# Kernel optimization log

Measured on AMD Instinct MI355X. Metric: run time of the kernel, lower is better.

The kernel has to match this reference:

```python
import jax, jax.numpy as jnp
import numpy as np

IN_F, H1, H2, OUT_F = 16, 512, 1024, 16
N_NODES, N_EDGES = 20000, 160000


def gcn_conv(x, src, dst, W, b, n):
    # PyG GCNConv: add self-loops, symmetric deg^-1/2 normalization,
    # linear transform first, then normalized scatter-add aggregation.
    loop = jnp.arange(n, dtype=src.dtype)
    s = jnp.concatenate([src, loop])
    d = jnp.concatenate([dst, loop])
    deg = jax.ops.segment_sum(jnp.ones(s.shape[0], x.dtype), d, num_segments=n)
    dinv = jnp.where(deg > 0, jax.lax.rsqrt(deg), 0.0)
    h = x @ W                      # [n, out]
    norm = dinv[s] * dinv[d]       # [e]
    msg = h[s] * norm[:, None]     # [e, out]
    return jax.ops.segment_sum(msg, d, num_segments=n) + b


def setup_inputs() -> dict:
    key = jax.random.key(0)
    ks = jax.random.split(key, 8)
    node_matrix = jax.random.normal(ks[0], (N_NODES, IN_F), dtype=jnp.float32)
    graph = jax.random.randint(ks[1], (2, N_EDGES), 0, N_NODES, dtype=jnp.int64)
    def glorot(k, shape):
        lim = np.sqrt(6.0 / (shape[0] + shape[1]))
        return jax.random.uniform(k, shape, jnp.float32, -lim, lim)
    return {
        "node_matrix": node_matrix,
        "graph": graph,
        "W1": glorot(ks[2], (IN_F, H1)),
        "b1": jnp.zeros((H1,), jnp.float32),
        "W2": glorot(ks[3], (H1, H2)),
        "b2": jnp.zeros((H2,), jnp.float32),
        "Wl": glorot(ks[4], (H2, OUT_F)),
        "bl": jnp.zeros((OUT_F,), jnp.float32),
    }


def reference(node_matrix, graph, W1, b1, W2, b2, Wl, bl):
    n = node_matrix.shape[0]
    src, dst = graph[0], graph[1]
    x = gcn_conv(node_matrix, src, dst, W1, b1, n)
    x = jax.nn.relu(x)
    # dropout is identity in eval mode
    x = gcn_conv(x, src, dst, W2, b2, n)
    return x @ Wl + bl
```

## Files before the change

### kernel.cpp

```cpp
#include <hip/hip_runtime.h>


constexpr int IN_F  = 16;
constexpr int H1D   = 512;
constexpr int H2D   = 1024;
constexpr int OUTF  = 16;
constexpr int PAD   = 64;

__global__ void k_prep(int* __restrict__ counts, float* __restrict__ WfB,
                       float* __restrict__ bf, float* __restrict__ W1T,
                       const float* __restrict__ W1, const float* __restrict__ W2,
                       const float* __restrict__ Wl, const float* __restrict__ b2,
                       const float* __restrict__ bl, int n) {
  int b = blockIdx.x, tid = threadIdx.x;
  if (b < 32) {
    int g = b * 256 + tid;
    int j = g >> 4, o = g & 15;
    const float* w2r = W2 + (size_t)j * H2D;
    float a0 = 0.f, a1 = 0.f, a2 = 0.f, a3 = 0.f;
#pragma unroll 4
    for (int k = 0; k < H2D; k += 4) {
      a0 = fmaf(w2r[k + 0], Wl[(k + 0) * OUTF + o], a0);
      a1 = fmaf(w2r[k + 1], Wl[(k + 1) * OUTF + o], a1);
      a2 = fmaf(w2r[k + 2], Wl[(k + 2) * OUTF + o], a2);
      a3 = fmaf(w2r[k + 3], Wl[(k + 3) * OUTF + o], a3);
    }
    WfB[j * OUTF + o] = (a0 + a1) + (a2 + a3);
  } else if (b < 64) {
    int t = (b - 32) * 256 + tid;
    int j = t >> 4, k = t & 15;
    W1T[t] = W1[k * H1D + j];
  } else if (b == 64) {
    if (tid < OUTF) {
      float a0 = 0.f, a1 = 0.f, a2 = 0.f, a3 = 0.f;
      for (int k = 0; k < H2D; k += 4) {
        a0 = fmaf(b2[k + 0], Wl[(k + 0) * OUTF + tid], a0);
        a1 = fmaf(b2[k + 1], Wl[(k + 1) * OUTF + tid], a1);
        a2 = fmaf(b2[k + 2], Wl[(k + 2) * OUTF + tid], a2);
        a3 = fmaf(b2[k + 3], Wl[(k + 3) * OUTF + tid], a3);
      }
      bf[tid] = bl[tid] + (a0 + a1) + (a2 + a3);
    }
  } else {
    int i = (b - 65) * 256 + tid;
    if (i < n) counts[i] = 0;
  }
}

__global__ void k_fill(const int* __restrict__ src, const int* __restrict__ dst,
                       int* __restrict__ counts, int* __restrict__ ell, int e) {
  int t = blockIdx.x * blockDim.x + threadIdx.x;
  if (t < e) {
    int d = dst[t];
    int slot = atomicAdd(&counts[d], 1);
    if (slot < PAD) ell[(size_t)d * PAD + slot] = src[t];
  }
}

__global__ __launch_bounds__(256) void k_gather(const float* __restrict__ V,
                                                const int* __restrict__ ell,
                                                const int* __restrict__ counts,
                                                const float* __restrict__ bias,
                                                float* __restrict__ O, int n) {
  int t = blockIdx.x * 256 + threadIdx.x;
  if (t >= n * 4) return;
  int i = t >> 2, q = t & 3;
  int cnt = counts[i];
  float di = rsqrtf(1.0f + (float)cnt);
  if (cnt > PAD) cnt = PAD;
  float4 acc = ((const float4*)(V + (size_t)i * 16))[q];
  acc.x *= di; acc.y *= di; acc.z *= di; acc.w *= di;
  const int* row = ell + (size_t)i * PAD;
  for (int k = 0; k < cnt; ++k) {
    int s = row[k];
    float ds = rsqrtf(1.0f + (float)counts[s]);
    float4 v = ((const float4*)(V + (size_t)s * 16))[q];
    acc.x = fmaf(v.x, ds, acc.x);
    acc.y = fmaf(v.y, ds, acc.y);
    acc.z = fmaf(v.z, ds, acc.z);
    acc.w = fmaf(v.w, ds, acc.w);
  }
  float4 o;
  if (bias) {
    float4 bq = ((const float4*)bias)[q];
    o = make_float4(fmaf(acc.x, di, bq.x), fmaf(acc.y, di, bq.y),
                    fmaf(acc.z, di, bq.z), fmaf(acc.w, di, bq.w));
  } else {
    o = make_float4(acc.x * di, acc.y * di, acc.z * di, acc.w * di);
  }
  ((float4*)O)[(size_t)i * 4 + q] = o;
}

template <int JC>
__global__ __launch_bounds__(256) void k_mlp_part(const float* __restrict__ Xa,
                                                  const float* __restrict__ W1T,
                                                  const float* __restrict__ b1,
                                                  const float* __restrict__ WfB,
                                                  float* __restrict__ part, int n) {
  int i = blockIdx.x * 256 + threadIdx.x;
  int c = blockIdx.y;
  bool valid = (i < n);
  int is = valid ? i : 0;

  float x[16];
  const float4* xr = (const float4*)(Xa + (size_t)is * 16);
#pragma unroll
  for (int q = 0; q < 4; ++q) {
    float4 v = xr[q];
    x[q * 4 + 0] = v.x; x[q * 4 + 1] = v.y; x[q * 4 + 2] = v.z; x[q * 4 + 3] = v.w;
  }

  float a[16];
#pragma unroll
  for (int o = 0; o < 16; ++o) a[o] = 0.f;

  const float* w1p = W1T + (size_t)c * JC * 16;
  const float* wfp = WfB + (size_t)c * JC * 16;
  const float* b1p = b1 + (size_t)c * JC;

#pragma unroll 4
  for (int jj = 0; jj < JC; ++jj) {
    const float* w1r = w1p + jj * 16;
    const float* wfr = wfp + jj * 16;
    float h0 = b1p[jj], h1 = 0.f, h2 = 0.f, h3 = 0.f;
#pragma unroll
    for (int k = 0; k < 4; ++k) {
      h0 = fmaf(x[k +  0], w1r[k +  0], h0);
      h1 = fmaf(x[k +  4], w1r[k +  4], h1);
      h2 = fmaf(x[k +  8], w1r[k +  8], h2);
      h3 = fmaf(x[k + 12], w1r[k + 12], h3);
    }
    float h = fmaxf((h0 + h1) + (h2 + h3), 0.f);
#pragma unroll
    for (int o = 0; o < 16; ++o) a[o] = fmaf(h, wfr[o], a[o]);
  }

  if (valid) {
    float4* pr = (float4*)(part + ((size_t)c * n + i) * 16);
#pragma unroll
    for (int q = 0; q < 4; ++q)
      pr[q] = make_float4(a[q * 4 + 0], a[q * 4 + 1], a[q * 4 + 2], a[q * 4 + 3]);
  }
}

__global__ void k_comb(const float* __restrict__ part, float* __restrict__ G,
                       int n, int C) {
  int t = blockIdx.x * blockDim.x + threadIdx.x;
  if (t < n * 4) {
    const float4* p = (const float4*)part;
    size_t stride = (size_t)n * 4;
    float4 s = p[t];
    for (int c = 1; c < C; ++c) {
      float4 v = p[(size_t)c * stride + t];
      s.x += v.x; s.y += v.y; s.z += v.z; s.w += v.w;
    }
    ((float4*)G)[t] = s;
  }
}

extern "C" void kernel_launch(void* const* d_in, const int* in_sizes, int n_in,
                              void* d_out, int out_size, void* d_ws, size_t ws_size,
                              hipStream_t stream) {
  (void)n_in; (void)out_size;
  const float* X   = (const float*)d_in[0];
  const int*   gr  = (const int*)d_in[1];
  const float* W1  = (const float*)d_in[2];
  const float* b1  = (const float*)d_in[3];
  const float* W2  = (const float*)d_in[4];
  const float* b2  = (const float*)d_in[5];
  const float* Wl  = (const float*)d_in[6];
  const float* bl  = (const float*)d_in[7];

  int n = in_sizes[0] / IN_F;
  int e = in_sizes[1] / 2;
  const int* src = gr;
  const int* dst = gr + e;

  float* ws   = (float*)d_ws;
  float* Xa   = ws;
  float* G    = Xa + (size_t)n * 16;
  float* WfB  = G + (size_t)n * 16;
  float* bf   = WfB + OUTF * H1D;
  float* W1T  = bf + 16;
  int*   counts = (int*)(W1T + IN_F * H1D);
  int*   ell    = counts + n;
  float* part   = (float*)(ell + (size_t)n * PAD);
  float* out  = (float*)d_out;

  size_t used = (size_t)((char*)part - (char*)ws);
  int C = 8;
  while (C > 1 && used + (size_t)C * n * 16 * 4 > ws_size) C >>= 1;

  const int TPB = 256;
  int nb_n  = (n + TPB - 1) / TPB;
  int nb_e  = (e + TPB - 1) / TPB;
  int nb_n4 = (n * 4 + TPB - 1) / TPB;

  k_prep<<<65 + nb_n, TPB, 0, stream>>>(counts, WfB, bf, W1T, W1, W2, Wl, b2, bl, n);
  k_fill<<<nb_e, TPB, 0, stream>>>(src, dst, counts, ell, e);

  k_gather<<<nb_n4, TPB, 0, stream>>>(X, ell, counts, nullptr, Xa, n);

  dim3 mg(nb_n, C);
  switch (C) {
    case 8: k_mlp_part<H1D / 8><<<mg, TPB, 0, stream>>>(Xa, W1T, b1, WfB, part, n); break;
    case 4: k_mlp_part<H1D / 4><<<mg, TPB, 0, stream>>>(Xa, W1T, b1, WfB, part, n); break;
    case 2: k_mlp_part<H1D / 2><<<mg, TPB, 0, stream>>>(Xa, W1T, b1, WfB, part, n); break;
    default: k_mlp_part<H1D><<<mg, TPB, 0, stream>>>(Xa, W1T, b1, WfB, part, n); break;
  }
  k_comb<<<nb_n4, TPB, 0, stream>>>(part, G, n, C);

  k_gather<<<nb_n4, TPB, 0, stream>>>(G, ell, counts, bf, out, n);
}
```

Before: 152.9 us.

## Fuse MLP chunk partials and combine into one kernel via shared-memory reduction

The split-K MLP previously wrote eight partial outputs per node to global memory and then ran a separate combine kernel to sum them. Now each 512-thread block handles 64 nodes, with its 8 wavefront groups each covering one hidden-dimension chunk. The partials are reduced in padded shared memory and written straight to G. This removes the partial-buffer write/read traffic and one launch, but costs a block-wide barrier, about 35KB of LDS per block, and fewer blocks (313).

```diff
diff --git a/kernel.cpp b/kernel.cpp
--- a/kernel.cpp
+++ b/kernel.cpp
@@ -6,6 +6,8 @@
 constexpr int H2D   = 1024;
 constexpr int OUTF  = 16;
 constexpr int PAD   = 64;
+constexpr int MLP_C = 8;
+constexpr int MLP_J = H1D / MLP_C;
 
 __global__ void k_prep(int* __restrict__ counts, float* __restrict__ WfB,
                        float* __restrict__ bf, float* __restrict__ W1T,
@@ -91,16 +93,17 @@
   ((float4*)O)[(size_t)i * 4 + q] = o;
 }
 
-template <int JC>
-__global__ __launch_bounds__(256) void k_mlp_part(const float* __restrict__ Xa,
-                                                  const float* __restrict__ W1T,
-                                                  const float* __restrict__ b1,
-                                                  const float* __restrict__ WfB,
-                                                  float* __restrict__ part, int n) {
-  int i = blockIdx.x * 256 + threadIdx.x;
-  int c = blockIdx.y;
-  bool valid = (i < n);
-  int is = valid ? i : 0;
+__global__ __launch_bounds__(512) void k_mlp(const float* __restrict__ Xa,
+                                             const float* __restrict__ W1T,
+                                             const float* __restrict__ b1,
+                                             const float* __restrict__ WfB,
+                                             float* __restrict__ G, int n) {
+  __shared__ float sred[MLP_C * 64 * 17];
+  int tid = threadIdx.x;
+  int c  = tid >> 6;
+  int nl = tid & 63;
+  int i  = blockIdx.x * 64 + nl;
+  int is = (i < n) ? i : 0;
 
   float x[16];
   const float4* xr = (const float4*)(Xa + (size_t)is * 16);
@@ -114,12 +117,12 @@
 #pragma unroll
   for (int o = 0; o < 16; ++o) a[o] = 0.f;
 
-  const float* w1p = W1T + (size_t)c * JC * 16;
-  const float* wfp = WfB + (size_t)c * JC * 16;
-  const float* b1p = b1 + (size_t)c * JC;
+  const float* w1p = W1T + c * MLP_J * 16;
+  const float* wfp = WfB + c * MLP_J * 16;
+  const float* b1p = b1 + c * MLP_J;
 
 #pragma unroll 4
-  for (int jj = 0; jj < JC; ++jj) {
+  for (int jj = 0; jj < MLP_J; ++jj) {
     const float* w1r = w1p + jj * 16;
     const float* wfr = wfp + jj * 16;
     float h0 = b1p[jj], h1 = 0.f, h2 = 0.f, h3 = 0.f;
@@ -135,33 +138,28 @@
     for (int o = 0; o < 16; ++o) a[o] = fmaf(h, wfr[o], a[o]);
   }
 
-  if (valid) {
-    float4* pr = (float4*)(part + ((size_t)c * n + i) * 16);
+  float* my = &sred[(c * 64 + nl) * 17];
 #pragma unroll
-    for (int q = 0; q < 4; ++q)
-      pr[q] = make_float4(a[q * 4 + 0], a[q * 4 + 1], a[q * 4 + 2], a[q * 4 + 3]);
-  }
-}
+  for (int o = 0; o < 16; ++o) my[o] = a[o];
+  __syncthreads();
 
-__global__ void k_comb(const float* __restrict__ part, float* __restrict__ G,
-                       int n, int C) {
-  int t = blockIdx.x * blockDim.x + threadIdx.x;
-  if (t < n * 4) {
-    const float4* p = (const float4*)part;
-    size_t stride = (size_t)n * 4;
-    float4 s = p[t];
-    for (int c = 1; c < C; ++c) {
-      float4 v = p[(size_t)c * stride + t];
-      s.x += v.x; s.y += v.y; s.z += v.z; s.w += v.w;
+#pragma unroll
+  for (int r = tid; r < 64 * 16; r += 512) {
+    int nl2 = r >> 4, o = r & 15;
+    int ii = blockIdx.x * 64 + nl2;
+    if (ii < n) {
+      float s = 0.f;
+#pragma unroll
+      for (int cc = 0; cc < MLP_C; ++cc) s += sred[(cc * 64 + nl2) * 17 + o];
+      G[(size_t)ii * 16 + o] = s;
     }
-    ((float4*)G)[t] = s;
   }
 }
 
 extern "C" void kernel_launch(void* const* d_in, const int* in_sizes, int n_in,
                               void* d_out, int out_size, void* d_ws, size_t ws_size,
                               hipStream_t stream) {
-  (void)n_in; (void)out_size;
+  (void)n_in; (void)out_size; (void)ws_size;
   const float* X   = (const float*)d_in[0];
   const int*   gr  = (const int*)d_in[1];
   const float* W1  = (const float*)d_in[2];
@@ -184,31 +182,17 @@
   float* W1T  = bf + 16;
   int*   counts = (int*)(W1T + IN_F * H1D);
   int*   ell    = counts + n;
-  float* part   = (float*)(ell + (size_t)n * PAD);
   float* out  = (float*)d_out;
-
-  size_t used = (size_t)((char*)part - (char*)ws);
-  int C = 8;
-  while (C > 1 && used + (size_t)C * n * 16 * 4 > ws_size) C >>= 1;
 
   const int TPB = 256;
   int nb_n  = (n + TPB - 1) / TPB;
   int nb_e  = (e + TPB - 1) / TPB;
   int nb_n4 = (n * 4 + TPB - 1) / TPB;
+  int nb_m  = (n + 63) / 64;
 
   k_prep<<<65 + nb_n, TPB, 0, stream>>>(counts, WfB, bf, W1T, W1, W2, Wl, b2, bl, n);
   k_fill<<<nb_e, TPB, 0, stream>>>(src, dst, counts, ell, e);
-
   k_gather<<<nb_n4, TPB, 0, stream>>>(X, ell, counts, nullptr, Xa, n);
-
-  dim3 mg(nb_n, C);
-  switch (C) {
-    case 8: k_mlp_part<H1D / 8><<<mg, TPB, 0, stream>>>(Xa, W1T, b1, WfB, part, n); break;
-    case 4: k_mlp_part<H1D / 4><<<mg, TPB, 0, stream>>>(Xa, W1T, b1, WfB, part, n); break;
-    case 2: k_mlp_part<H1D / 2><<<mg, TPB, 0, stream>>>(Xa, W1T, b1, WfB, part, n); break;
-    default: k_mlp_part<H1D><<<mg, TPB, 0, stream>>>(Xa, W1T, b1, WfB, part, n); break;
-  }
-  k_comb<<<nb_n4, TPB, 0, stream>>>(part, G, n, C);
-
+  k_mlp<<<nb_m, 512, 0, stream>>>(Xa, W1T, b1, WfB, G, n);
   k_gather<<<nb_n4, TPB, 0, stream>>>(G, ell, counts, bf, out, n);
 }
```

Result: slower. 186.8 us (+22.1%).
